# Optimization experiments

Measured on AMD Instinct MI355X. Metric: run time of the kernel, lower is better.

## Reference

```python
import jax, jax.numpy as jnp
import numpy as np

D_MODEL = 1024
NHEAD = 16
HEAD_DIM = D_MODEL // NHEAD


def setup_inputs() -> dict:
    key = jax.random.key(0)
    ks = jax.random.split(key, 11)
    B, S, D = 4, 2048, D_MODEL
    scale = 1.0 / np.sqrt(D)
    inp = {
        'q': jax.random.normal(ks[0], (B, S, D), jnp.float32),
        'k': jax.random.normal(ks[1], (B, S, D), jnp.float32),
        'v': jax.random.normal(ks[2], (B, S, D), jnp.float32),
        'Wq': jax.random.normal(ks[3], (D, D), jnp.float32) * scale,
        'bq': jnp.zeros((D,), jnp.float32),
        'Wk': jax.random.normal(ks[4], (D, D), jnp.float32) * scale,
        'bk': jnp.zeros((D,), jnp.float32),
        'Wv': jax.random.normal(ks[5], (D, D), jnp.float32) * scale,
        'bv': jnp.zeros((D,), jnp.float32),
        'Wo': jax.random.normal(ks[6], (D, D), jnp.float32) * scale,
        'bo': jnp.zeros((D,), jnp.float32),
    }
    return inp


def reference(q, k, v, Wq, bq, Wk, bk, Wv, bv, Wo, bo):
    B, S, D = q.shape
    H, Hd = NHEAD, HEAD_DIM
    # projections (torch Linear: x @ W.T + b), then split heads -> [B,H,S,Hd]
    qh = (q @ Wq.T + bq).reshape(B, S, H, Hd).transpose(0, 2, 1, 3)
    kh = (k @ Wk.T + bk).reshape(B, S, H, Hd).transpose(0, 2, 1, 3)
    vh = (v @ Wv.T + bv).reshape(B, S, H, Hd).transpose(0, 2, 1, 3)
    # scaled dot-product attention (mask=None, dropout eval-mode identity)
    scores = jnp.einsum('bhqd,bhkd->bhqk', qh, kh) / jnp.sqrt(jnp.float32(Hd))
    attn = jax.nn.softmax(scores, axis=-1)
    out = jnp.einsum('bhqk,bhkd->bhqd', attn, vh)  # [B,H,S,Hd]
    out = out.transpose(0, 2, 1, 3).reshape(B, S, D)
    return out @ Wo.T + bo
```

## Files before the change

kernel.cpp:

```cpp
#include <hip/hip_runtime.h>
#include <cstdint>

using u16 = unsigned short;
using u32 = unsigned int;
typedef __bf16 bf16x8 __attribute__((ext_vector_type(8)));
typedef float f32x4 __attribute__((ext_vector_type(4)));
typedef float f32x16 __attribute__((ext_vector_type(16)));
typedef u16 u16x8 __attribute__((ext_vector_type(8)));
typedef u16 u16x4 __attribute__((ext_vector_type(4)));

#define DEV static __device__ __forceinline__

DEV u16 f2bf(float f) {
  uint32_t u = __builtin_bit_cast(uint32_t, f);
  u += 0x7FFFu + ((u >> 16) & 1u);
  return (u16)(u >> 16);
}
DEV float bf2f(u16 h) {
  uint32_t u = ((uint32_t)h) << 16;
  return __builtin_bit_cast(float, u);
}
DEV u32 cvt_pk_bf16(float lo, float hi) {
  u32 r;
  asm("v_cvt_pk_bf16_f32 %0, %1, %2" : "=v"(r) : "v"(lo), "v"(hi));
  return r;
}

typedef const u32 __attribute__((address_space(1))) gcu32;
typedef u32 __attribute__((address_space(3))) lu32;
DEV void gl_lds16(const u16* g, u16* l) {
  __builtin_amdgcn_global_load_lds((gcu32*)g, (lu32*)l, 16, 0, 0);
}

#define MFMA(a, b, c) __builtin_amdgcn_mfma_f32_16x16x32_bf16((a), (b), (c), 0, 0, 0)
#define MFMA32(a, b, c) __builtin_amdgcn_mfma_f32_32x32x16_bf16((a), (b), (c), 0, 0, 0)

#define WAITV(n) asm volatile("s_waitcnt vmcnt(" #n ")" ::: "memory")

__global__ __launch_bounds__(256) void cvt_all(
    const float* __restrict__ q, const float* __restrict__ k,
    const float* __restrict__ v, const float* __restrict__ Wq,
    const float* __restrict__ Wk, const float* __restrict__ Wv,
    const float* __restrict__ Wo, u16* __restrict__ Xb, u16* __restrict__ Wb,
    u16* __restrict__ WoB) {
  const int bid = blockIdx.x;
  const float* src;
  u16* dst;
  size_t i;
  if (bid < 12288) {
    const int z = bid >> 12;
    src = (z == 0) ? q : (z == 1) ? k : v;
    dst = Xb + (size_t)z * 8388608;
    i = ((size_t)(bid & 4095) * 256 + threadIdx.x) * 8;
  } else {
    const int r = bid - 12288;
    const int z = r >> 9;
    src = (z == 0) ? Wq : (z == 1) ? Wk : (z == 2) ? Wv : Wo;
    dst = (z < 3) ? (Wb + (size_t)z * 1048576) : WoB;
    i = ((size_t)(r & 511) * 256 + threadIdx.x) * 8;
  }
  const float4 a = *(const float4*)(src + i);
  const float4 b = *(const float4*)(src + i + 4);
  u16x8 o;
  o[0] = f2bf(a.x); o[1] = f2bf(a.y); o[2] = f2bf(a.z); o[3] = f2bf(a.w);
  o[4] = f2bf(b.x); o[5] = f2bf(b.y); o[6] = f2bf(b.z); o[7] = f2bf(b.w);
  *(u16x8*)(dst + i) = o;
}

__global__ __launch_bounds__(256) void proj_gemm_bf(
    const u16* __restrict__ Xb, const u16* __restrict__ Wb,
    const float* __restrict__ bq, const float* __restrict__ bk,
    const float* __restrict__ bv, u16* __restrict__ Qh, u16* __restrict__ Kh,
    u16* __restrict__ Vt) {
  __shared__ u16 As[2][128 * 64];
  __shared__ u16 Bs[2][128 * 64];
  const int z = blockIdx.z;
  const int m0 = blockIdx.x * 128, n0 = blockIdx.y * 128;

  const u16* x = Xb + (size_t)z * 8388608;
  const u16* W = Wb + (size_t)z * 1048576;
  const float* bias = (z == 0) ? bq : (z == 1) ? bk : bv;
  u16* out = (z == 0) ? Qh : (z == 1) ? Kh : Vt;
  const float oscale = (z == 0) ? 0.18033688011112042f : 1.0f;

  const int tid = threadIdx.x;
  const int w = tid >> 6, lane = tid & 63;
  const int wr = w >> 1, wc = w & 1;
  const int lr = lane & 15, hq = lane >> 4;

  const int srow = w * 8 + (lane >> 3);
  const int scol = ((lane & 7) ^ ((lane >> 3) & 7)) * 8;
  const u16* xg = x + (size_t)(m0 + srow) * 1024 + scol;
  const u16* wg_ = W + (size_t)(n0 + srow) * 1024 + scol;

  f32x4 acc[4][4];
  const f32x4 fzero = {0.f, 0.f, 0.f, 0.f};
#pragma unroll
  for (int m = 0; m < 4; ++m)
#pragma unroll
    for (int n = 0; n < 4; ++n) acc[m][n] = fzero;

#define PSTAGE(b, t)                                                          \
  {                                                                           \
    _Pragma("unroll") for (int c = 0; c < 4; ++c) {                           \
      gl_lds16(xg + (size_t)c * 32 * 1024 + (t) * 64,                         \
               &As[b][c * 2048 + w * 512]);                                   \
      gl_lds16(wg_ + (size_t)c * 32 * 1024 + (t) * 64,                        \
               &Bs[b][c * 2048 + w * 512]);                                   \
    }                                                                         \
  }

  PSTAGE(0, 0);

#pragma unroll
  for (int t = 0; t < 16; ++t) {
    const int cur = t & 1;
    if (t < 15) {
      PSTAGE(cur ^ 1, t + 1);
      WAITV(8);
    } else {
      WAITV(0);
    }
    __builtin_amdgcn_s_barrier();
    __builtin_amdgcn_sched_barrier(0);
    __builtin_amdgcn_s_setprio(1);
#pragma unroll
    for (int kk = 0; kk < 2; ++kk) {
      bf16x8 a[4], b[4];
#pragma unroll
      for (int m = 0; m < 4; ++m) {
        const int row = wr * 64 + m * 16 + lr;
        a[m] = *(const bf16x8*)&As[cur][row * 64 + (((kk * 4 + hq) ^ (lr & 7)) * 8)];
      }
#pragma unroll
      for (int n = 0; n < 4; ++n) {
        const int row = wc * 64 + n * 16 + lr;
        b[n] = *(const bf16x8*)&Bs[cur][row * 64 + (((kk * 4 + hq) ^ (lr & 7)) * 8)];
      }
#pragma unroll
      for (int m = 0; m < 4; ++m)
#pragma unroll
        for (int n = 0; n < 4; ++n) acc[m][n] = MFMA(a[m], b[n], acc[m][n]);
    }
    __builtin_amdgcn_s_setprio(0);
    __builtin_amdgcn_sched_barrier(0);
    __builtin_amdgcn_s_barrier();
  }
#undef PSTAGE

#pragma unroll
  for (int n = 0; n < 4; ++n) {
    const int col = n0 + wc * 64 + n * 16 + lr;
    const float bvv = bias[col];
    const int h = col >> 6, d = col & 63;
#pragma unroll
    for (int m = 0; m < 4; ++m) {
#pragma unroll
      for (int j = 0; j < 4; ++j) {
        const int rowg = m0 + wr * 64 + m * 16 + hq * 4 + j;
        const int bb = rowg >> 11, s = rowg & 2047;
        const float val = (acc[m][n][j] + bvv) * oscale;
        size_t idx;
        if (z != 2)
          idx = ((size_t)(bb * 16 + h) * 2048 + s) * 64 + d;
        else
          idx = ((size_t)(bb * 16 + h) * 64 + d) * 2048 + s;
        out[idx] = f2bf(val);
      }
    }
  }
}

__global__ __launch_bounds__(256) void proj_gemm_f32(
    const float* __restrict__ q, const float* __restrict__ k,
    const float* __restrict__ v, const float* __restrict__ Wq,
    const float* __restrict__ Wk, const float* __restrict__ Wv,
    const float* __restrict__ bq, const float* __restrict__ bk,
    const float* __restrict__ bv, u16* __restrict__ Qh, u16* __restrict__ Kh,
    u16* __restrict__ Vt) {
  __shared__ u16 As[128][40];
  __shared__ u16 Bs[128][40];
  const int z = blockIdx.z;
  const float* x = (z == 0) ? q : (z == 1) ? k : v;
  const float* W = (z == 0) ? Wq : (z == 1) ? Wk : Wv;
  const float* bias = (z == 0) ? bq : (z == 1) ? bk : bv;
  u16* out = (z == 0) ? Qh : (z == 1) ? Kh : Vt;
  const float oscale = (z == 0) ? 0.18033688011112042f : 1.0f;

  const int tid = threadIdx.x;
  const int m0 = blockIdx.y * 128, n0 = blockIdx.x * 128;
  const int w = tid >> 6, lane = tid & 63;
  const int wr = w >> 1, wc = w & 1;
  const int lr = lane & 15, lk = (lane >> 4) * 8;
  const int srow = tid >> 3, sc4 = (tid & 7) * 4;

  f32x4 acc[4][4];
  const f32x4 fzero = {0.f, 0.f, 0.f, 0.f};
#pragma unroll
  for (int m = 0; m < 4; ++m)
#pragma unroll
    for (int n = 0; n < 4; ++n) acc[m][n] = fzero;

  for (int kt = 0; kt < 32; ++kt) {
    const int k0 = kt * 32;
    __syncthreads();
#pragma unroll
    for (int c = 0; c < 4; ++c) {
      const float4 av = *(const float4*)(x + (size_t)(m0 + c * 32 + srow) * 1024 + k0 + sc4);
      const float4 bvv = *(const float4*)(W + (size_t)(n0 + c * 32 + srow) * 1024 + k0 + sc4);
      u16x4 ah, bh;
      ah[0] = f2bf(av.x); ah[1] = f2bf(av.y); ah[2] = f2bf(av.z); ah[3] = f2bf(av.w);
      bh[0] = f2bf(bvv.x); bh[1] = f2bf(bvv.y); bh[2] = f2bf(bvv.z); bh[3] = f2bf(bvv.w);
      *(u16x4*)&As[c * 32 + srow][sc4] = ah;
      *(u16x4*)&Bs[c * 32 + srow][sc4] = bh;
    }
    __syncthreads();
    bf16x8 a[4], b[4];
#pragma unroll
    for (int m = 0; m < 4; ++m)
      a[m] = *(const bf16x8*)&As[wr * 64 + m * 16 + lr][lk];
#pragma unroll
    for (int n = 0; n < 4; ++n)
      b[n] = *(const bf16x8*)&Bs[wc * 64 + n * 16 + lr][lk];
#pragma unroll
    for (int m = 0; m < 4; ++m)
#pragma unroll
      for (int n = 0; n < 4; ++n) acc[m][n] = MFMA(a[m], b[n], acc[m][n]);
  }

#pragma unroll
  for (int n = 0; n < 4; ++n) {
    const int col = n0 + wc * 64 + n * 16 + lr;
    const float bvv = bias[col];
    const int h = col >> 6, d = col & 63;
#pragma unroll
    for (int m = 0; m < 4; ++m) {
#pragma unroll
      for (int j = 0; j < 4; ++j) {
        const int rowg = m0 + wr * 64 + m * 16 + (lane >> 4) * 4 + j;
        const int bb = rowg >> 11, s = rowg & 2047;
        const float val = (acc[m][n][j] + bvv) * oscale;
        size_t idx;
        if (z != 2)
          idx = ((size_t)(bb * 16 + h) * 2048 + s) * 64 + d;
        else
          idx = ((size_t)(bb * 16 + h) * 64 + d) * 2048 + s;
        out[idx] = f2bf(val);
      }
    }
  }
}

__global__ __launch_bounds__(512, 4) void attn_fwd(
    const u16* __restrict__ Qh, const u16* __restrict__ Kh,
    const u16* __restrict__ Vt, u16* __restrict__ Att) {
  __shared__ u16 Ks[64][72];
  __shared__ u16 Vs[64][72];
  const int tid = threadIdx.x;
  const int w = tid >> 6, lane = tid & 63;
  const int lq = lane & 31, h = lane >> 5;
  const int head = blockIdx.x, q0 = blockIdx.y * 256;
  const u16* Qb = Qh + (size_t)head * 131072;
  const u16* Kb = Kh + (size_t)head * 131072;
  const u16* Vb = Vt + (size_t)head * 131072;
  const int qrow = q0 + w * 32 + lq;

  bf16x8 qf[4];
#pragma unroll
  for (int dc = 0; dc < 4; ++dc)
    qf[dc] = *(const bf16x8*)(Qb + (size_t)qrow * 64 + dc * 16 + h * 8);

  u16x8 ou;
#pragma unroll
  for (int j = 0; j < 8; ++j) ou[j] = 0x3F80;
  const bf16x8 ones = __builtin_bit_cast(bf16x8, ou);

  f32x16 o0 = {}, o1 = {}, osum = {};

  const int srow = tid >> 3, scol = (tid & 7) * 8;
  uint4 kr, vr;
  kr = *(const uint4*)(Kb + (size_t)srow * 64 + scol);
  vr = *(const uint4*)(Vb + (size_t)srow * 2048 + scol);

  for (int kt = 0; kt < 32; ++kt) {
    __syncthreads();
    *(uint4*)&Ks[srow][scol] = kr;
    *(uint4*)&Vs[srow][scol] = vr;
    __syncthreads();
    if (kt + 1 < 32) {
      const int t0n = (kt + 1) * 64;
      kr = *(const uint4*)(Kb + (size_t)(t0n + srow) * 64 + scol);
      vr = *(const uint4*)(Vb + (size_t)srow * 2048 + t0n + scol);
    }

    f32x16 s0 = {}, s1 = {};
    __builtin_amdgcn_s_setprio(1);
#pragma unroll
    for (int dc = 0; dc < 4; ++dc) {
      const bf16x8 k0 = *(const bf16x8*)&Ks[lq][dc * 16 + h * 8];
      const bf16x8 k1 = *(const bf16x8*)&Ks[32 + lq][dc * 16 + h * 8];
      s0 = MFMA32(k0, qf[dc], s0);
      s1 = MFMA32(k1, qf[dc], s1);
    }
    __builtin_amdgcn_s_setprio(0);

#pragma unroll
    for (int r = 0; r < 16; ++r) {
      s0[r] = __builtin_amdgcn_exp2f(s0[r]);
      s1[r] = __builtin_amdgcn_exp2f(s1[r]);
    }

    u32 w0[8], w1[8];
#pragma unroll
    for (int b = 0; b < 4; ++b)
#pragma unroll
      for (int e = 0; e < 2; ++e) {
        w0[b * 2 + e] = cvt_pk_bf16(s0[4 * b + 2 * e], s0[4 * b + 2 * e + 1]);
        w1[b * 2 + e] = cvt_pk_bf16(s1[4 * b + 2 * e], s1[4 * b + 2 * e + 1]);
      }

    bf16x8 pa[4];
#pragma unroll
    for (int c = 0; c < 2; ++c) {
      u32 a0 = w0[(2 * c) * 2 + 0], b0 = w0[(2 * c + 1) * 2 + 0];
      u32 a1 = w0[(2 * c) * 2 + 1], b1 = w0[(2 * c + 1) * 2 + 1];
      asm("v_permlane32_swap_b32 %0, %1" : "+v"(a0), "+v"(b0));
      asm("v_permlane32_swap_b32 %0, %1" : "+v"(a1), "+v"(b1));
      const uint4 f = {a0, a1, b0, b1};
      pa[c] = __builtin_bit_cast(bf16x8, f);
    }
#pragma unroll
    for (int c = 0; c < 2; ++c) {
      u32 a0 = w1[(2 * c) * 2 + 0], b0 = w1[(2 * c + 1) * 2 + 0];
      u32 a1 = w1[(2 * c) * 2 + 1], b1 = w1[(2 * c + 1) * 2 + 1];
      asm("v_permlane32_swap_b32 %0, %1" : "+v"(a0), "+v"(b0));
      asm("v_permlane32_swap_b32 %0, %1" : "+v"(a1), "+v"(b1));
      const uint4 f = {a0, a1, b0, b1};
      pa[2 + c] = __builtin_bit_cast(bf16x8, f);
    }

    __builtin_amdgcn_s_setprio(1);
#pragma unroll
    for (int c = 0; c < 4; ++c) {
      const bf16x8 v0f = *(const bf16x8*)&Vs[lq][c * 16 + h * 8];
      const bf16x8 v1f = *(const bf16x8*)&Vs[32 + lq][c * 16 + h * 8];
      o0 = MFMA32(pa[c], v0f, o0);
      o1 = MFMA32(pa[c], v1f, o1);
      osum = MFMA32(pa[c], ones, osum);
    }
    __builtin_amdgcn_s_setprio(0);
  }

  const int bb = head >> 4, hh = head & 15;
#pragma unroll
  for (int r = 0; r < 16; ++r) {
    const int qr = (r & 3) + 8 * (r >> 2) + 4 * h;
    const float li = 1.0f / osum[r];
    const int qg = q0 + w * 32 + qr;
    const size_t base = ((size_t)(bb * 2048 + qg)) * 1024 + hh * 64;
    Att[base + lq] = f2bf(o0[r] * li);
    Att[base + 32 + lq] = f2bf(o1[r] * li);
  }
}

__global__ __launch_bounds__(256) void out_gemm_bf(
    const u16* __restrict__ Att, const u16* __restrict__ WoB,
    const float* __restrict__ bo, float* __restrict__ out) {
  __shared__ u16 As[2][128 * 64];
  __shared__ u16 Bs[2][128 * 64];
  const int m0 = blockIdx.x * 128, n0 = blockIdx.y * 128;
  const int tid = threadIdx.x;
  const int w = tid >> 6, lane = tid & 63;
  const int wr = w >> 1, wc = w & 1;
  const int lr = lane & 15, hq = lane >> 4;

  const int srow = w * 8 + (lane >> 3);
  const int scol = ((lane & 7) ^ ((lane >> 3) & 7)) * 8;
  const u16* ag = Att + (size_t)(m0 + srow) * 1024 + scol;
  const u16* bg = WoB + (size_t)(n0 + srow) * 1024 + scol;

  f32x4 acc[4][4];
  const f32x4 fzero = {0.f, 0.f, 0.f, 0.f};
#pragma unroll
  for (int m = 0; m < 4; ++m)
#pragma unroll
    for (int n = 0; n < 4; ++n) acc[m][n] = fzero;

#define OSTAGE(b, t)                                                          \
  {                                                                           \
    _Pragma("unroll") for (int c = 0; c < 4; ++c) {                           \
      gl_lds16(ag + (size_t)c * 32 * 1024 + (t) * 64,                         \
               &As[b][c * 2048 + w * 512]);                                   \
      gl_lds16(bg + (size_t)c * 32 * 1024 + (t) * 64,                         \
               &Bs[b][c * 2048 + w * 512]);                                   \
    }                                                                         \
  }

  OSTAGE(0, 0);

#pragma unroll
  for (int t = 0; t < 16; ++t) {
    const int cur = t & 1;
    if (t < 15) {
      OSTAGE(cur ^ 1, t + 1);
      WAITV(8);
    } else {
      WAITV(0);
    }
    __builtin_amdgcn_s_barrier();
    __builtin_amdgcn_sched_barrier(0);
    __builtin_amdgcn_s_setprio(1);
#pragma unroll
    for (int kk = 0; kk < 2; ++kk) {
      bf16x8 a[4], b[4];
#pragma unroll
      for (int m = 0; m < 4; ++m) {
        const int row = wr * 64 + m * 16 + lr;
        a[m] = *(const bf16x8*)&As[cur][row * 64 + (((kk * 4 + hq) ^ (lr & 7)) * 8)];
      }
#pragma unroll
      for (int n = 0; n < 4; ++n) {
        const int row = wc * 64 + n * 16 + lr;
        b[n] = *(const bf16x8*)&Bs[cur][row * 64 + (((kk * 4 + hq) ^ (lr & 7)) * 8)];
      }
#pragma unroll
      for (int m = 0; m < 4; ++m)
#pragma unroll
        for (int n = 0; n < 4; ++n) acc[m][n] = MFMA(a[m], b[n], acc[m][n]);
    }
    __builtin_amdgcn_s_setprio(0);
    __builtin_amdgcn_sched_barrier(0);
    __builtin_amdgcn_s_barrier();
  }
#undef OSTAGE

#pragma unroll
  for (int n = 0; n < 4; ++n) {
    const int col = n0 + wc * 64 + n * 16 + lr;
    const float bvv = bo[col];
#pragma unroll
    for (int m = 0; m < 4; ++m)
#pragma unroll
      for (int j = 0; j < 4; ++j) {
        const int rowg = m0 + wr * 64 + m * 16 + hq * 4 + j;
        out[(size_t)rowg * 1024 + col] = acc[m][n][j] + bvv;
      }
  }
}

__global__ __launch_bounds__(256) void out_gemm_f32(
    const u16* __restrict__ Att, const float* __restrict__ Wo,
    const float* __restrict__ bo, float* __restrict__ out) {
  __shared__ u16 As[128][40], Bs[128][40];
  const int tid = threadIdx.x;
  const int m0 = blockIdx.y * 128, n0 = blockIdx.x * 128;
  const int w = tid >> 6, lane = tid & 63;
  const int wr = w >> 1, wc = w & 1;
  const int lr = lane & 15, lk = (lane >> 4) * 8;
  const int arow = tid >> 2, ac8 = (tid & 3) * 8;
  const int wrow = tid >> 3, wc4 = (tid & 7) * 4;

  f32x4 acc[4][4];
  const f32x4 fzero = {0.f, 0.f, 0.f, 0.f};
#pragma unroll
  for (int m = 0; m < 4; ++m)
#pragma unroll
    for (int n = 0; n < 4; ++n) acc[m][n] = fzero;

  for (int kt = 0; kt < 32; ++kt) {
    const int k0 = kt * 32;
    __syncthreads();
#pragma unroll
    for (int c = 0; c < 2; ++c) {
      *(uint4*)&As[c * 64 + arow][ac8] =
          *(const uint4*)(Att + (size_t)(m0 + c * 64 + arow) * 1024 + k0 + ac8);
    }
#pragma unroll
    for (int c = 0; c < 4; ++c) {
      const float4 wv = *(const float4*)(Wo + (size_t)(n0 + c * 32 + wrow) * 1024 + k0 + wc4);
      u16x4 hv;
      hv[0] = f2bf(wv.x); hv[1] = f2bf(wv.y); hv[2] = f2bf(wv.z); hv[3] = f2bf(wv.w);
      *(u16x4*)&Bs[c * 32 + wrow][wc4] = hv;
    }
    __syncthreads();
    bf16x8 a[4], b[4];
#pragma unroll
    for (int m = 0; m < 4; ++m)
      a[m] = *(const bf16x8*)&As[wr * 64 + m * 16 + lr][lk];
#pragma unroll
    for (int n = 0; n < 4; ++n)
      b[n] = *(const bf16x8*)&Bs[wc * 64 + n * 16 + lr][lk];
#pragma unroll
    for (int m = 0; m < 4; ++m)
#pragma unroll
      for (int n = 0; n < 4; ++n) acc[m][n] = MFMA(a[m], b[n], acc[m][n]);
  }

#pragma unroll
  for (int n = 0; n < 4; ++n) {
    const int col = n0 + wc * 64 + n * 16 + lr;
    const float bvv = bo[col];
#pragma unroll
    for (int m = 0; m < 4; ++m)
#pragma unroll
      for (int j = 0; j < 4; ++j) {
        const int rowg = m0 + wr * 64 + m * 16 + (lane >> 4) * 4 + j;
        out[(size_t)rowg * 1024 + col] = acc[m][n][j] + bvv;
      }
  }
}

extern "C" void kernel_launch(void* const* d_in, const int* in_sizes, int n_in,
                              void* d_out, int out_size, void* d_ws, size_t ws_size,
                              hipStream_t stream) {
  const float* q  = (const float*)d_in[0];
  const float* k  = (const float*)d_in[1];
  const float* v  = (const float*)d_in[2];
  const float* Wq = (const float*)d_in[3];
  const float* bq = (const float*)d_in[4];
  const float* Wk = (const float*)d_in[5];
  const float* bk = (const float*)d_in[6];
  const float* Wv = (const float*)d_in[7];
  const float* bv = (const float*)d_in[8];
  const float* Wo = (const float*)d_in[9];
  const float* bo = (const float*)d_in[10];

  u16* ws  = (u16*)d_ws;
  u16* Qh  = ws;
  u16* Kh  = ws + (size_t)8388608;
  u16* Vt  = ws + (size_t)16777216;
  u16* Att = ws + (size_t)25165824;
  u16* Xb  = ws + (size_t)25165824;
  u16* Wb  = ws + (size_t)50331648;
  u16* WoB = ws + (size_t)53477376;
  const size_t need = (size_t)55574528 * 2;

  if (ws_size >= need) {
    cvt_all<<<dim3(14336), dim3(256), 0, stream>>>(q, k, v, Wq, Wk, Wv, Wo, Xb,
                                                   Wb, WoB);
    proj_gemm_bf<<<dim3(64, 8, 3), dim3(256), 0, stream>>>(Xb, Wb, bq, bk, bv,
                                                           Qh, Kh, Vt);
    attn_fwd<<<dim3(64, 8), dim3(512), 0, stream>>>(Qh, Kh, Vt, Att);
    out_gemm_bf<<<dim3(64, 8), dim3(256), 0, stream>>>(Att, WoB, bo,
                                                       (float*)d_out);
  } else {
    proj_gemm_f32<<<dim3(8, 64, 3), dim3(256), 0, stream>>>(
        q, k, v, Wq, Wk, Wv, bq, bk, bv, Qh, Kh, Vt);
    attn_fwd<<<dim3(64, 8), dim3(512), 0, stream>>>(Qh, Kh, Vt, Att);
    out_gemm_f32<<<dim3(8, 64), dim3(256), 0, stream>>>(Att, Wo, bo,
                                                        (float*)d_out);
  }
}
```

Baseline: 193.7 us.

## Double attention KV tile per sync and compute row sums with VALU instead of MFMA

Each loop iteration now stages 128 keys and values instead of 64, halving the number of barrier-synchronised iterations and prefetch rounds. The softmax denominator is accumulated as a per-lane scalar sum of the fp32 exponentials plus a cross-half shuffle, replacing the extra MFMA against a ones vector. This removes a third of the PV MFMAs and half the barriers, but doubles LDS use per block and adds VALU adds and shuffles. The row sum now uses the unrounded fp32 values rather than the bf16-rounded probabilities, which changes numerics slightly.

```diff
diff --git a/kernel.cpp b/kernel.cpp
--- a/kernel.cpp
+++ b/kernel.cpp
@@ -254,8 +254,8 @@
 __global__ __launch_bounds__(512, 4) void attn_fwd(
     const u16* __restrict__ Qh, const u16* __restrict__ Kh,
     const u16* __restrict__ Vt, u16* __restrict__ Att) {
-  __shared__ u16 Ks[64][72];
-  __shared__ u16 Vs[64][72];
+  __shared__ u16 Ks[128][72];
+  __shared__ u16 Vs[64][136];
   const int tid = threadIdx.x;
   const int w = tid >> 6, lane = tid & 63;
   const int lq = lane & 31, h = lane >> 5;
@@ -270,92 +270,105 @@
   for (int dc = 0; dc < 4; ++dc)
     qf[dc] = *(const bf16x8*)(Qb + (size_t)qrow * 64 + dc * 16 + h * 8);
 
-  u16x8 ou;
-#pragma unroll
-  for (int j = 0; j < 8; ++j) ou[j] = 0x3F80;
-  const bf16x8 ones = __builtin_bit_cast(bf16x8, ou);
-
-  f32x16 o0 = {}, o1 = {}, osum = {};
+  f32x16 o0 = {}, o1 = {};
+  float lsum = 0.f;
 
   const int srow = tid >> 3, scol = (tid & 7) * 8;
-  uint4 kr, vr;
-  kr = *(const uint4*)(Kb + (size_t)srow * 64 + scol);
-  vr = *(const uint4*)(Vb + (size_t)srow * 2048 + scol);
-
-  for (int kt = 0; kt < 32; ++kt) {
+  uint4 kr0, kr1, vr0, vr1;
+  kr0 = *(const uint4*)(Kb + (size_t)srow * 64 + scol);
+  kr1 = *(const uint4*)(Kb + (size_t)(64 + srow) * 64 + scol);
+  vr0 = *(const uint4*)(Vb + (size_t)srow * 2048 + scol);
+  vr1 = *(const uint4*)(Vb + (size_t)srow * 2048 + 64 + scol);
+
+  for (int kt = 0; kt < 16; ++kt) {
     __syncthreads();
-    *(uint4*)&Ks[srow][scol] = kr;
-    *(uint4*)&Vs[srow][scol] = vr;
+    *(uint4*)&Ks[srow][scol] = kr0;
+    *(uint4*)&Ks[64 + srow][scol] = kr1;
+    *(uint4*)&Vs[srow][scol] = vr0;
+    *(uint4*)&Vs[srow][64 + scol] = vr1;
     __syncthreads();
-    if (kt + 1 < 32) {
-      const int t0n = (kt + 1) * 64;
-      kr = *(const uint4*)(Kb + (size_t)(t0n + srow) * 64 + scol);
-      vr = *(const uint4*)(Vb + (size_t)srow * 2048 + t0n + scol);
-    }
-
-    f32x16 s0 = {}, s1 = {};
-    __builtin_amdgcn_s_setprio(1);
-#pragma unroll
-    for (int dc = 0; dc < 4; ++dc) {
-      const bf16x8 k0 = *(const bf16x8*)&Ks[lq][dc * 16 + h * 8];
-      const bf16x8 k1 = *(const bf16x8*)&Ks[32 + lq][dc * 16 + h * 8];
-      s0 = MFMA32(k0, qf[dc], s0);
-      s1 = MFMA32(k1, qf[dc], s1);
-    }
-    __builtin_amdgcn_s_setprio(0);
-
-#pragma unroll
-    for (int r = 0; r < 16; ++r) {
-      s0[r] = __builtin_amdgcn_exp2f(s0[r]);
-      s1[r] = __builtin_amdgcn_exp2f(s1[r]);
-    }
-
-    u32 w0[8], w1[8];
-#pragma unroll
-    for (int b = 0; b < 4; ++b)
-#pragma unroll
-      for (int e = 0; e < 2; ++e) {
-        w0[b * 2 + e] = cvt_pk_bf16(s0[4 * b + 2 * e], s0[4 * b + 2 * e + 1]);
-        w1[b * 2 + e] = cvt_pk_bf16(s1[4 * b + 2 * e], s1[4 * b + 2 * e + 1]);
-      }
-
-    bf16x8 pa[4];
-#pragma unroll
-    for (int c = 0; c < 2; ++c) {
-      u32 a0 = w0[(2 * c) * 2 + 0], b0 = w0[(2 * c + 1) * 2 + 0];
-      u32 a1 = w0[(2 * c) * 2 + 1], b1 = w0[(2 * c + 1) * 2 + 1];
-      asm("v_permlane32_swap_b32 %0, %1" : "+v"(a0), "+v"(b0));
-      asm("v_permlane32_swap_b32 %0, %1" : "+v"(a1), "+v"(b1));
-      const uint4 f = {a0, a1, b0, b1};
-      pa[c] = __builtin_bit_cast(bf16x8, f);
-    }
-#pragma unroll
-    for (int c = 0; c < 2; ++c) {
-      u32 a0 = w1[(2 * c) * 2 + 0], b0 = w1[(2 * c + 1) * 2 + 0];
-      u32 a1 = w1[(2 * c) * 2 + 1], b1 = w1[(2 * c + 1) * 2 + 1];
-      asm("v_permlane32_swap_b32 %0, %1" : "+v"(a0), "+v"(b0));
-      asm("v_permlane32_swap_b32 %0, %1" : "+v"(a1), "+v"(b1));
-      const uint4 f = {a0, a1, b0, b1};
-      pa[2 + c] = __builtin_bit_cast(bf16x8, f);
-    }
-
-    __builtin_amdgcn_s_setprio(1);
-#pragma unroll
-    for (int c = 0; c < 4; ++c) {
-      const bf16x8 v0f = *(const bf16x8*)&Vs[lq][c * 16 + h * 8];
-      const bf16x8 v1f = *(const bf16x8*)&Vs[32 + lq][c * 16 + h * 8];
-      o0 = MFMA32(pa[c], v0f, o0);
-      o1 = MFMA32(pa[c], v1f, o1);
-      osum = MFMA32(pa[c], ones, osum);
-    }
-    __builtin_amdgcn_s_setprio(0);
-  }
+    if (kt + 1 < 16) {
+      const int t0n = (kt + 1) * 128;
+      kr0 = *(const uint4*)(Kb + (size_t)(t0n + srow) * 64 + scol);
+      kr1 = *(const uint4*)(Kb + (size_t)(t0n + 64 + srow) * 64 + scol);
+      vr0 = *(const uint4*)(Vb + (size_t)srow * 2048 + t0n + scol);
+      vr1 = *(const uint4*)(Vb + (size_t)srow * 2048 + t0n + 64 + scol);
+    }
+
+#pragma unroll
+    for (int half = 0; half < 2; ++half) {
+      const int ko = half * 64;
+
+      f32x16 s0 = {}, s1 = {};
+      __builtin_amdgcn_s_setprio(1);
+#pragma unroll
+      for (int dc = 0; dc < 4; ++dc) {
+        const bf16x8 k0 = *(const bf16x8*)&Ks[ko + lq][dc * 16 + h * 8];
+        const bf16x8 k1 = *(const bf16x8*)&Ks[ko + 32 + lq][dc * 16 + h * 8];
+        s0 = MFMA32(k0, qf[dc], s0);
+        s1 = MFMA32(k1, qf[dc], s1);
+      }
+      __builtin_amdgcn_s_setprio(0);
+
+      float rs = 0.f;
+#pragma unroll
+      for (int r = 0; r < 16; ++r) {
+        s0[r] = __builtin_amdgcn_exp2f(s0[r]);
+        s1[r] = __builtin_amdgcn_exp2f(s1[r]);
+        rs += s0[r];
+        rs += s1[r];
+      }
+      lsum += rs;
+
+      u32 w0[8], w1[8];
+#pragma unroll
+      for (int b = 0; b < 4; ++b)
+#pragma unroll
+        for (int e = 0; e < 2; ++e) {
+          w0[b * 2 + e] = cvt_pk_bf16(s0[4 * b + 2 * e], s0[4 * b + 2 * e + 1]);
+          w1[b * 2 + e] = cvt_pk_bf16(s1[4 * b + 2 * e], s1[4 * b + 2 * e + 1]);
+        }
+
+      bf16x8 pa[4];
+#pragma unroll
+      for (int c = 0; c < 2; ++c) {
+        u32 a0 = w0[(2 * c) * 2 + 0], b0 = w0[(2 * c + 1) * 2 + 0];
+        u32 a1 = w0[(2 * c) * 2 + 1], b1 = w0[(2 * c + 1) * 2 + 1];
+        asm("v_permlane32_swap_b32 %0, %1" : "+v"(a0), "+v"(b0));
+        asm("v_permlane32_swap_b32 %0, %1" : "+v"(a1), "+v"(b1));
+        const uint4 f = {a0, a1, b0, b1};
+        pa[c] = __builtin_bit_cast(bf16x8, f);
+      }
+#pragma unroll
+      for (int c = 0; c < 2; ++c) {
+        u32 a0 = w1[(2 * c) * 2 + 0], b0 = w1[(2 * c + 1) * 2 + 0];
+        u32 a1 = w1[(2 * c) * 2 + 1], b1 = w1[(2 * c + 1) * 2 + 1];
+        asm("v_permlane32_swap_b32 %0, %1" : "+v"(a0), "+v"(b0));
+        asm("v_permlane32_swap_b32 %0, %1" : "+v"(a1), "+v"(b1));
+        const uint4 f = {a0, a1, b0, b1};
+        pa[2 + c] = __builtin_bit_cast(bf16x8, f);
+      }
+
+      __builtin_amdgcn_s_setprio(1);
+#pragma unroll
+      for (int c = 0; c < 4; ++c) {
+        const bf16x8 v0f = *(const bf16x8*)&Vs[lq][ko + c * 16 + h * 8];
+        const bf16x8 v1f = *(const bf16x8*)&Vs[32 + lq][ko + c * 16 + h * 8];
+        o0 = MFMA32(pa[c], v0f, o0);
+        o1 = MFMA32(pa[c], v1f, o1);
+      }
+      __builtin_amdgcn_s_setprio(0);
+    }
+  }
+
+  lsum += __shfl_xor(lsum, 32);
 
   const int bb = head >> 4, hh = head & 15;
+  const float linv = 1.0f / lsum;
 #pragma unroll
   for (int r = 0; r < 16; ++r) {
     const int qr = (r & 3) + 8 * (r >> 2) + 4 * h;
-    const float li = 1.0f / osum[r];
+    const float li = __shfl(linv, qr);
     const int qg = q0 + w * 32 + qr;
     const size_t base = ((size_t)(bb * 2048 + qg)) * 1024 + hh * 64;
     Att[base + lq] = f2bf(o0[r] * li);
```

Result: no change. 191.3 us (median of 5 runs) (-1.3%).
